# Kernel tuning notes

Hardware: AMD Instinct MI355X
Metric: run time of the kernel (lower is better)

The kernel has to match this reference:

```python
import jax, jax.numpy as jnp
import numpy as np

DT = 0.01
M = 1.0
G = 9.81
K_DRAG = 0.05


def setup_inputs() -> dict:
    key = jax.random.key(0)
    k1, k2 = jax.random.split(key)
    B = 2_000_000
    state = jax.random.normal(k1, (B, 12), dtype=jnp.float32)
    u = jax.random.uniform(k2, (B, 4), dtype=jnp.float32)
    I = jnp.array([0.01, 0.01, 0.02], dtype=jnp.float32)
    g_vec = jnp.array([0.0, 0.0, -M * G], dtype=jnp.float32)
    return {"state": state, "u": u, "I": I, "g_vec": g_vec}


def _dynamics(state, u, I, g_vec):
    # state: (B, 12) = [pos(3), vel(3), att(3), omega(3)]; u: (B, 4) = [T, Mx, My, Mz]
    vel = state[:, 3:6]
    att = state[:, 6:9]
    omega = state[:, 9:12]
    roll, pitch, yaw = att[:, 0], att[:, 1], att[:, 2]
    c_r, s_r = jnp.cos(roll), jnp.sin(roll)
    c_p, s_p = jnp.cos(pitch), jnp.sin(pitch)
    c_y, s_y = jnp.cos(yaw), jnp.sin(yaw)

    # body->world rotation matrix, built row-wise: (B, 3, 3)
    row0 = jnp.stack([c_y * c_p, c_y * s_p * s_r - s_y * c_r, c_y * s_p * c_r + s_y * s_r], axis=1)
    row1 = jnp.stack([s_y * c_p, s_y * s_p * s_r + c_y * c_r, s_y * s_p * c_r - c_y * s_r], axis=1)
    row2 = jnp.stack([-s_p, c_p * s_r, c_p * c_r], axis=1)
    R = jnp.stack([row0, row1, row2], axis=1)

    v_norm = jnp.maximum(jnp.linalg.norm(vel, axis=1, keepdims=True), 1e-8)
    drag = -K_DRAG * v_norm * vel

    # thrust in body frame is [0, 0, T]; R @ [0,0,T] == T * R[:, :, 2]
    thrust_world = R[:, :, 2] * u[:, 0:1]
    acc = (thrust_world + drag + g_vec[None, :]) / M

    tau = u[:, 1:4]
    Ib = I[None, :]
    omega_cross = jnp.cross(omega, omega * Ib)
    omega_dot = (tau - omega_cross) / Ib

    c_pitch = jnp.where(jnp.abs(c_p) < 1e-6, jnp.full_like(c_p, 1e-6), c_p)
    t_pitch = s_p / c_pitch
    roll_dot = omega[:, 0] + s_r * t_pitch * omega[:, 1] + c_r * t_pitch * omega[:, 2]
    pitch_dot = c_r * omega[:, 1] - s_r * omega[:, 2]
    yaw_dot = s_r / c_pitch * omega[:, 1] + c_r / c_pitch * omega[:, 2]
    att_dot = jnp.stack([roll_dot, pitch_dot, yaw_dot], axis=1)

    return jnp.concatenate([vel, acc, att_dot, omega_dot], axis=1)


def reference(state, u, I, g_vec):
    # RK4 single step
    k1 = _dynamics(state, u, I, g_vec)
    k2 = _dynamics(state + 0.5 * DT * k1, u, I, g_vec)
    k3 = _dynamics(state + 0.5 * DT * k2, u, I, g_vec)
    k4 = _dynamics(state + DT * k3, u, I, g_vec)
    return state + DT / 6.0 * (k1 + 2 * k2 + 2 * k3 + k4)
```

## Files before the change

kernel.cpp:

```cpp
#include <hip/hip_runtime.h>
#include <math.h>

#define DT_F        ((float)0.01)
#define HALF_DT_F   ((float)(0.5 * 0.01))
#define DT6_F       ((float)(0.01 / 6.0))
#define K_DRAG_F    ((float)0.05)
#define INV_2PI_F   0.15915494309189535f
#define BLOCK 256

__device__ __forceinline__ void hw_sincos(float a, float* s, float* c) {
    const float r = a * INV_2PI_F;
    *s = __builtin_amdgcn_sinf(r);
    *c = __builtin_amdgcn_cosf(r);
}

__device__ __forceinline__ void dyn(const float* __restrict__ s,
                                    float u0, float tx, float ty, float tz,
                                    float iI0, float iI1, float iI2,
                                    float I0, float I1, float I2,
                                    float gx, float gy, float gz,
                                    float* __restrict__ k)
{
    const float vx = s[3], vy = s[4], vz = s[5];
    const float roll = s[6], pitch = s[7], yaw = s[8];
    const float wx = s[9], wy = s[10], wz = s[11];

    float s_r, c_r, s_p, c_p, s_y, c_y;
    hw_sincos(roll, &s_r, &c_r);
    sincosf(pitch, &s_p, &c_p);
    hw_sincos(yaw,  &s_y, &c_y);

    const float spcr = s_p * c_r;
    const float r02 = c_y * spcr + s_y * s_r;
    const float r12 = s_y * spcr - c_y * s_r;
    const float r22 = c_p * c_r;

    float vn = __builtin_amdgcn_sqrtf(vx * vx + vy * vy + vz * vz);
    vn = fmaxf(vn, 1e-8f);
    const float dscale = -K_DRAG_F * vn;

    const float ax = r02 * u0 + dscale * vx + gx;
    const float ay = r12 * u0 + dscale * vy + gy;
    const float az = r22 * u0 + dscale * vz + gz;

    const float bx = wx * I0, by = wy * I1, bz = wz * I2;
    const float cx = wy * bz - wz * by;
    const float cy = wz * bx - wx * bz;
    const float cz = wx * by - wy * bx;
    const float wdx = (tx - cx) * iI0;
    const float wdy = (ty - cy) * iI1;
    const float wdz = (tz - cz) * iI2;

    const float c_pitch = (fabsf(c_p) < 1e-6f) ? 1e-6f : c_p;
    const float inv_cp = __builtin_amdgcn_rcpf(c_pitch);
    const float t_pitch = s_p * inv_cp;
    const float roll_dot  = wx + s_r * t_pitch * wy + c_r * t_pitch * wz;
    const float pitch_dot = c_r * wy - s_r * wz;
    const float yaw_dot   = (s_r * inv_cp) * wy + (c_r * inv_cp) * wz;

    k[0] = vx;  k[1] = vy;  k[2] = vz;
    k[3] = ax;  k[4] = ay;  k[5] = az;
    k[6] = roll_dot; k[7] = pitch_dot; k[8] = yaw_dot;
    k[9] = wdx; k[10] = wdy; k[11] = wdz;
}

__global__ __launch_bounds__(BLOCK)
void drone_rk4_kernel(const float* __restrict__ state,
                      const float* __restrict__ u,
                      const float* __restrict__ I,
                      const float* __restrict__ g,
                      float* __restrict__ out, int B)
{
    __shared__ float4 lds[BLOCK * 3];

    const int t = threadIdx.x;
    const long long base = (long long)blockIdx.x * BLOCK;
    const long long nvec = (long long)B * 3;
    const bool valid = (base + t) < B;

    const float4* sv = reinterpret_cast<const float4*>(state);
    #pragma unroll
    for (int r = 0; r < 3; ++r) {
        const long long f = base * 3 + r * BLOCK + t;
        if (f < nvec) lds[r * BLOCK + t] = sv[f];
    }
    __syncthreads();

    const float4 a0 = lds[t * 3 + 0];
    const float4 a1 = lds[t * 3 + 1];
    const float4 a2 = lds[t * 3 + 2];
    __syncthreads();

    float s0[12] = {a0.x, a0.y, a0.z, a0.w,
                    a1.x, a1.y, a1.z, a1.w,
                    a2.x, a2.y, a2.z, a2.w};

    float4 uu = make_float4(0.f, 0.f, 0.f, 0.f);
    if (valid) uu = reinterpret_cast<const float4*>(u)[base + t];

    const float I0 = I[0], I1 = I[1], I2 = I[2];
    const float gx = g[0], gy = g[1], gz = g[2];
    const float iI0 = __builtin_amdgcn_rcpf(I0);
    const float iI1 = __builtin_amdgcn_rcpf(I1);
    const float iI2 = __builtin_amdgcn_rcpf(I2);

    float k1[12], k2[12], k3[12], k4[12], tmp[12];

    dyn(s0, uu.x, uu.y, uu.z, uu.w, iI0, iI1, iI2, I0, I1, I2, gx, gy, gz, k1);
    #pragma unroll
    for (int j = 0; j < 12; ++j) tmp[j] = fmaf(HALF_DT_F, k1[j], s0[j]);
    dyn(tmp, uu.x, uu.y, uu.z, uu.w, iI0, iI1, iI2, I0, I1, I2, gx, gy, gz, k2);
    #pragma unroll
    for (int j = 0; j < 12; ++j) tmp[j] = fmaf(HALF_DT_F, k2[j], s0[j]);
    dyn(tmp, uu.x, uu.y, uu.z, uu.w, iI0, iI1, iI2, I0, I1, I2, gx, gy, gz, k3);
    #pragma unroll
    for (int j = 0; j < 12; ++j) tmp[j] = fmaf(DT_F, k3[j], s0[j]);
    dyn(tmp, uu.x, uu.y, uu.z, uu.w, iI0, iI1, iI2, I0, I1, I2, gx, gy, gz, k4);

    float o[12];
    #pragma unroll
    for (int j = 0; j < 12; ++j)
        o[j] = s0[j] + DT6_F * (k1[j] + 2.0f * k2[j] + 2.0f * k3[j] + k4[j]);

    lds[t * 3 + 0] = make_float4(o[0], o[1], o[2],  o[3]);
    lds[t * 3 + 1] = make_float4(o[4], o[5], o[6],  o[7]);
    lds[t * 3 + 2] = make_float4(o[8], o[9], o[10], o[11]);
    __syncthreads();

    float4* ov = reinterpret_cast<float4*>(out);
    #pragma unroll
    for (int r = 0; r < 3; ++r) {
        const long long f = base * 3 + r * BLOCK + t;
        if (f < nvec) ov[f] = lds[r * BLOCK + t];
    }
}

extern "C" void kernel_launch(void* const* d_in, const int* in_sizes, int n_in,
                              void* d_out, int out_size, void* d_ws, size_t ws_size,
                              hipStream_t stream)
{
    const float* state = (const float*)d_in[0];
    const float* u     = (const float*)d_in[1];
    const float* I     = (const float*)d_in[2];
    const float* g     = (const float*)d_in[3];
    float* out = (float*)d_out;

    const int B = in_sizes[0] / 12;
    const int grid = (B + BLOCK - 1) / BLOCK;
    drone_rk4_kernel<<<grid, BLOCK, 0, stream>>>(state, u, I, g, out, B);
}
```

Measured before the change: 197.0 us.

## Process four drones per thread with direct strided float4 loads, dropping LDS staging

Each thread now handles four drones. It issues all of their state and control loads up front, then runs RK4 on each and writes the results straight to global memory. The shared-memory transpose and its barriers are gone, which removes the LDS round trip and sync cost and puts more memory requests in flight per thread. In exchange, each thread's three float4 accesses hit strided addresses (48-byte stride), so coalescing is worse, and holding four drones of state raises register pressure, which may lower occupancy.

```diff
diff --git a/kernel.cpp b/kernel.cpp
--- a/kernel.cpp
+++ b/kernel.cpp
@@ -7,6 +7,7 @@
 #define K_DRAG_F    ((float)0.05)
 #define INV_2PI_F   0.15915494309189535f
 #define BLOCK 256
+#define DPT 4
 
 __device__ __forceinline__ void hw_sincos(float a, float* s, float* c) {
     const float r = a * INV_2PI_F;
@@ -64,46 +65,16 @@
     k[9] = wdx; k[10] = wdy; k[11] = wdz;
 }
 
-__global__ __launch_bounds__(BLOCK)
-void drone_rk4_kernel(const float* __restrict__ state,
-                      const float* __restrict__ u,
-                      const float* __restrict__ I,
-                      const float* __restrict__ g,
-                      float* __restrict__ out, int B)
+__device__ __forceinline__ void rk4_one(const float4& a0, const float4& a1,
+                                        const float4& a2, const float4& uu,
+                                        float iI0, float iI1, float iI2,
+                                        float I0, float I1, float I2,
+                                        float gx, float gy, float gz,
+                                        float4& o0, float4& o1, float4& o2)
 {
-    __shared__ float4 lds[BLOCK * 3];
-
-    const int t = threadIdx.x;
-    const long long base = (long long)blockIdx.x * BLOCK;
-    const long long nvec = (long long)B * 3;
-    const bool valid = (base + t) < B;
-
-    const float4* sv = reinterpret_cast<const float4*>(state);
-    #pragma unroll
-    for (int r = 0; r < 3; ++r) {
-        const long long f = base * 3 + r * BLOCK + t;
-        if (f < nvec) lds[r * BLOCK + t] = sv[f];
-    }
-    __syncthreads();
-
-    const float4 a0 = lds[t * 3 + 0];
-    const float4 a1 = lds[t * 3 + 1];
-    const float4 a2 = lds[t * 3 + 2];
-    __syncthreads();
-
     float s0[12] = {a0.x, a0.y, a0.z, a0.w,
                     a1.x, a1.y, a1.z, a1.w,
                     a2.x, a2.y, a2.z, a2.w};
-
-    float4 uu = make_float4(0.f, 0.f, 0.f, 0.f);
-    if (valid) uu = reinterpret_cast<const float4*>(u)[base + t];
-
-    const float I0 = I[0], I1 = I[1], I2 = I[2];
-    const float gx = g[0], gy = g[1], gz = g[2];
-    const float iI0 = __builtin_amdgcn_rcpf(I0);
-    const float iI1 = __builtin_amdgcn_rcpf(I1);
-    const float iI2 = __builtin_amdgcn_rcpf(I2);
-
     float k1[12], k2[12], k3[12], k4[12], tmp[12];
 
     dyn(s0, uu.x, uu.y, uu.z, uu.w, iI0, iI1, iI2, I0, I1, I2, gx, gy, gz, k1);
@@ -122,16 +93,59 @@
     for (int j = 0; j < 12; ++j)
         o[j] = s0[j] + DT6_F * (k1[j] + 2.0f * k2[j] + 2.0f * k3[j] + k4[j]);
 
-    lds[t * 3 + 0] = make_float4(o[0], o[1], o[2],  o[3]);
-    lds[t * 3 + 1] = make_float4(o[4], o[5], o[6],  o[7]);
-    lds[t * 3 + 2] = make_float4(o[8], o[9], o[10], o[11]);
-    __syncthreads();
+    o0 = make_float4(o[0], o[1], o[2],  o[3]);
+    o1 = make_float4(o[4], o[5], o[6],  o[7]);
+    o2 = make_float4(o[8], o[9], o[10], o[11]);
+}
+
+__global__ __launch_bounds__(BLOCK)
+void drone_rk4_kernel(const float* __restrict__ state,
+                      const float* __restrict__ u,
+                      const float* __restrict__ I,
+                      const float* __restrict__ g,
+                      float* __restrict__ out, int B)
+{
+    const int t = threadIdx.x;
+    const long long base = (long long)blockIdx.x * (BLOCK * DPT);
+
+    const float4* sv = reinterpret_cast<const float4*>(state);
+    const float4* uv = reinterpret_cast<const float4*>(u);
+
+    float4 st[DPT][3];
+    float4 uu[DPT];
+    long long idx[DPT];
+    bool valid[DPT];
+    #pragma unroll
+    for (int d = 0; d < DPT; ++d) {
+        idx[d] = base + d * BLOCK + t;
+        valid[d] = idx[d] < B;
+        const long long f = idx[d] * 3;
+        if (valid[d]) {
+            st[d][0] = sv[f + 0];
+            st[d][1] = sv[f + 1];
+            st[d][2] = sv[f + 2];
+            uu[d]    = uv[idx[d]];
+        }
+    }
+
+    const float I0 = I[0], I1 = I[1], I2 = I[2];
+    const float gx = g[0], gy = g[1], gz = g[2];
+    const float iI0 = __builtin_amdgcn_rcpf(I0);
+    const float iI1 = __builtin_amdgcn_rcpf(I1);
+    const float iI2 = __builtin_amdgcn_rcpf(I2);
 
     float4* ov = reinterpret_cast<float4*>(out);
+
     #pragma unroll
-    for (int r = 0; r < 3; ++r) {
-        const long long f = base * 3 + r * BLOCK + t;
-        if (f < nvec) ov[f] = lds[r * BLOCK + t];
+    for (int d = 0; d < DPT; ++d) {
+        if (!valid[d]) continue;
+        float4 o0, o1, o2;
+        rk4_one(st[d][0], st[d][1], st[d][2], uu[d],
+                iI0, iI1, iI2, I0, I1, I2, gx, gy, gz, o0, o1, o2);
+        const long long f = idx[d] * 3;
+        ov[f + 0] = o0;
+        ov[f + 1] = o1;
+        ov[f + 2] = o2;
     }
 }
 
@@ -146,6 +160,7 @@
     float* out = (float*)d_out;
 
     const int B = in_sizes[0] / 12;
-    const int grid = (B + BLOCK - 1) / BLOCK;
+    const int per_block = BLOCK * DPT;
+    const int grid = (B + per_block - 1) / per_block;
     drone_rk4_kernel<<<grid, BLOCK, 0, stream>>>(state, u, I, g, out, B);
 }
```

After: 205.1 us. +4.1%, slower.
